# Kernel tuning notes

Hardware: AMD Instinct MI355X
Metric: run time of the kernel (lower is better)

The kernel has to match this reference:

```python
import jax, jax.numpy as jnp
import numpy as np

NB, HD, NL, NF = 5, 64, 4, 10           # num_bins, hidden_dim(d_model), num_layers, num_frames
DI, DS, DC, DTR = 128, 16, 4, 4          # d_inner=2*HD, d_state, d_conv, dt_rank=ceil(HD/16)
B, H, W = 4, 64, 64


def _conv2d(x, w, b):
    y = jax.lax.conv_general_dilated(x, w, (1, 1), 'SAME',
                                     dimension_numbers=('NCHW', 'OIHW', 'NCHW'))
    return y + b[None, :, None, None]


def _bn_relu(x, gamma, beta, eps=1e-5):
    # BatchNorm2d in training mode: biased batch stats over (N,H,W)
    mean = x.mean(axis=(0, 2, 3), keepdims=True)
    var = x.var(axis=(0, 2, 3), keepdims=True)
    y = (x - mean) * jax.lax.rsqrt(var + eps)
    return jax.nn.relu(y * gamma[None, :, None, None] + beta[None, :, None, None])


def _silu(x):
    return x * jax.nn.sigmoid(x)


def _causal_dwconv(x, w, b):
    # x: (B,L,DI), w: (DI,K) depthwise causal conv, b: (DI,)
    K = w.shape[1]
    L = x.shape[1]
    xp = jnp.pad(x, ((0, 0), (K - 1, 0), (0, 0)))
    y = sum(xp[:, k:k + L, :] * w[:, k] for k in range(K))
    return y + b


def _selective_scan(u, delta, A, Bm, Cm, D):
    # u,delta: (B,L,DI); A: (DI,DS); Bm,Cm: (B,L,DS); D: (DI,)
    dT, BT, CT, uT = (t.transpose(1, 0, 2) for t in (delta, Bm, Cm, u))
    h0 = jnp.zeros((u.shape[0], A.shape[0], A.shape[1]), u.dtype)

    def step(h, inp):
        d_t, B_t, C_t, u_t = inp                     # (B,DI),(B,DS),(B,DS),(B,DI)
        dA = jnp.exp(d_t[:, :, None] * A)            # (B,DI,DS)
        h = dA * h + (d_t * u_t)[:, :, None] * B_t[:, None, :]
        y = jnp.einsum('bds,bs->bd', h, C_t)
        return h, y

    _, ys = jax.lax.scan(step, h0, (dT, BT, CT, uT))  # ys: (L,B,DI)
    return ys.transpose(1, 0, 2) + u * D


def _mamba(x, in_proj, conv_w, conv_b, x_proj, dt_w, dt_b, A_log, Dp, out_proj):
    xz = x @ in_proj.T                               # (B,L,2*DI)
    xi, z = jnp.split(xz, 2, axis=-1)
    xi = _silu(_causal_dwconv(xi, conv_w, conv_b))
    xdbc = xi @ x_proj.T                             # (B,L,DTR+2*DS)
    dt, Bm, Cm = jnp.split(xdbc, [DTR, DTR + DS], axis=-1)
    delta = jax.nn.softplus(dt @ dt_w.T + dt_b)
    A = -jnp.exp(A_log)
    y = _selective_scan(xi, delta, A, Bm, Cm, Dp)
    return (y * _silu(z)) @ out_proj.T


def setup_inputs() -> dict:
    key = jax.random.key(0)
    ks = jax.random.split(key, 20)
    s = 0.02
    inp = {
        'x': jax.random.normal(ks[0], (B, NB, H, W), jnp.float32),
        'enc_w': jax.random.normal(ks[1], (HD, NB, 3, 3), jnp.float32) * s,
        'enc_b': jnp.zeros((HD,), jnp.float32),
        'enc_g': jnp.ones((HD,), jnp.float32),
        'enc_be': jnp.zeros((HD,), jnp.float32),
        'in_proj': jax.random.normal(ks[2], (NL, 2 * DI, HD), jnp.float32) * s,
        'conv_w': jax.random.normal(ks[3], (NL, DI, DC), jnp.float32) * s,
        'conv_b': jnp.zeros((NL, DI), jnp.float32),
        'x_proj': jax.random.normal(ks[4], (NL, DTR + 2 * DS, DI), jnp.float32) * s,
        'dt_w': jax.random.normal(ks[5], (NL, DI, DTR), jnp.float32) * s,
        'dt_b': jax.random.normal(ks[6], (NL, DI), jnp.float32) * 0.1 - 4.0,
        'A_log': jnp.broadcast_to(jnp.log(jnp.arange(1, DS + 1, dtype=jnp.float32)),
                                  (NL, DI, DS)).copy(),
        'Dp': jnp.ones((NL, DI), jnp.float32),
        'out_proj': jax.random.normal(ks[7], (NL, HD, DI), jnp.float32) * s,
        'dec1_w': jax.random.normal(ks[8], (HD, HD, 3, 3), jnp.float32) * s,
        'dec1_b': jnp.zeros((HD,), jnp.float32),
        'dec1_g': jnp.ones((HD,), jnp.float32),
        'dec1_be': jnp.zeros((HD,), jnp.float32),
        'dec2_w': jax.random.normal(ks[9], (NF, HD, 3, 3), jnp.float32) * s,
        'dec2_b': jnp.zeros((NF,), jnp.float32),
    }
    return inp


def reference(x, enc_w, enc_b, enc_g, enc_be, in_proj, conv_w, conv_b, x_proj,
              dt_w, dt_b, A_log, Dp, out_proj, dec1_w, dec1_b, dec1_g, dec1_be,
              dec2_w, dec2_b):
    Bb, _, Hh, Ww = x.shape
    h = _bn_relu(_conv2d(x, enc_w, enc_b), enc_g, enc_be)   # (B,HD,H,W)
    t = h.reshape(Bb, HD, Hh * Ww).transpose(0, 2, 1)        # (B,L,HD)
    for i in range(NL):
        t = t + _mamba(t, in_proj[i], conv_w[i], conv_b[i], x_proj[i],
                       dt_w[i], dt_b[i], A_log[i], Dp[i], out_proj[i])
    h = t.transpose(0, 2, 1).reshape(Bb, HD, Hh, Ww)
    h = _bn_relu(_conv2d(h, dec1_w, dec1_b), dec1_g, dec1_be)
    return _conv2d(h, dec2_w, dec2_b)                        # (B,NF,H,W)
```

## Files before the change

kernel.cpp:

```cpp
#include <hip/hip_runtime.h>
#include <hip/hip_bf16.h>

#define BB   4
#define NBC  5
#define HD   64
#define NLAYER 4
#define NFC  10
#define DIM  128
#define DSN  16
#define DCN  4
#define DTRK 4
#define HH   64
#define WWD  64
#define LL   4096
#define MM   (BB*LL)
#define NCHUNK 128
#define CLEN   32
#define TSTEP  16

__global__ void k_prep_all(const float* __restrict__ in_proj, const float* __restrict__ out_proj,
                           const float* __restrict__ dec1_w, const float* __restrict__ dec2_w,
                           float* __restrict__ wTin, float* __restrict__ wTout,
                           float* __restrict__ wT1, float* __restrict__ wT2,
                           float* __restrict__ stats, float* __restrict__ stats2) {
    int idx = blockIdx.x * blockDim.x + threadIdx.x;
    if (idx < 65536) {
        int n = idx & 255, k = (idx >> 8) & 63, l = idx >> 14;
        wTin[idx] = in_proj[(l << 14) + (n << 6) + k];
    } else if (idx < 98304) {
        int j = idx - 65536;
        int n = j & 63, k = (j >> 6) & 127, l = j >> 13;
        wTout[j] = out_proj[(l << 13) + (n << 7) + k];
    } else if (idx < 135168) {
        int j = idx - 98304;
        int co = j & 63, tap = (j >> 6) % 9, ci = j / 576;
        wT1[j] = dec1_w[co * 576 + ci * 9 + tap];
    } else if (idx < 142848) {
        int j = idx - 135168;
        int tap = j % 12, t2 = j / 12, co = t2 % NFC, ci = t2 / NFC;
        wT2[j] = (tap < 9) ? dec2_w[co * 576 + ci * 9 + tap] : 0.f;
    } else if (idx < 143104) {
        int j = idx - 142848;
        if (j < 128) stats[j] = 0.f; else stats2[j - 128] = 0.f;
    }
}

__global__ void k_enc_conv(const float* __restrict__ x, const float* __restrict__ w,
                           const float* __restrict__ bias, float* __restrict__ out,
                           float* __restrict__ stats) {
    __shared__ float r1[256], r2[256];
    int tid = threadIdx.x;
    int idx = blockIdx.x * 256 + tid;
    int wx = idx & 63;
    int hy = (idx >> 6) & 63;
    int co = (idx >> 12) & 63;
    int b  = idx >> 18;
    float acc = bias[co];
    for (int ci = 0; ci < NBC; ++ci) {
        const float* xin = x + (((long)(b * NBC + ci)) << 12);
        const float* wp  = w + (co * NBC + ci) * 9;
        #pragma unroll
        for (int kh = 0; kh < 3; ++kh) {
            int ih = hy + kh - 1;
            if (ih < 0 || ih >= HH) continue;
            #pragma unroll
            for (int kw = 0; kw < 3; ++kw) {
                int iw = wx + kw - 1;
                if (iw < 0 || iw >= WWD) continue;
                acc += xin[(ih << 6) + iw] * wp[kh * 3 + kw];
            }
        }
    }
    out[idx] = acc;
    r1[tid] = acc; r2[tid] = acc * acc;
    __syncthreads();
    for (int off = 128; off > 0; off >>= 1) {
        if (tid < off) { r1[tid] += r1[tid + off]; r2[tid] += r2[tid + off]; }
        __syncthreads();
    }
    if (tid == 0) {
        atomicAdd(&stats[co], r1[0]);
        atomicAdd(&stats[64 + co], r2[0]);
    }
}

__global__ __launch_bounds__(256, 1) void k_gemm_in_bn(const float* __restrict__ src,
                                                       const float* __restrict__ stats,
                                                       const float* __restrict__ g,
                                                       const float* __restrict__ be,
                                                       const float* __restrict__ wT,
                                                       float* __restrict__ tout,
                                                       float* __restrict__ xz) {
    __shared__ __align__(16) float ts[64 * 68];
    __shared__ float sc[64], sh[64];
    long m0 = (long)blockIdx.x << 6;
    int b = (int)(m0 >> 12);
    int hw0 = (int)(m0 & 4095);
    int tid = threadIdx.x;
    if (tid < 64) {
        float m = stats[tid] * (1.f / 16384.f);
        float var = stats[64 + tid] * (1.f / 16384.f) - m * m;
        float ss = g[tid] * rsqrtf(var + 1e-5f);
        sc[tid] = ss; sh[tid] = be[tid] - m * ss;
    }
    __syncthreads();
    for (int i = tid; i < 4096; i += 256) {
        int pix = i & 63, c = i >> 6;
        float v = src[(((long)((b << 6) + c)) << 12) + hw0 + pix];
        ts[pix * 68 + c] = fmaxf(v * sc[c] + sh[c], 0.f);
    }
    __syncthreads();
    for (int i = tid; i < 4096; i += 256) {
        int r = i >> 6, c = i & 63;
        tout[(m0 + r) * 64 + c] = ts[r * 68 + c];
    }
    int rg = tid >> 5;
    int cg = tid & 31;
    float acc[8][8] = {};
    int n0 = cg << 3;
    for (int k4 = 0; k4 < 16; ++k4) {
        float4 a[8];
        #pragma unroll
        for (int r2 = 0; r2 < 8; ++r2)
            a[r2] = *(const float4*)&ts[((rg << 3) + r2) * 68 + (k4 << 2)];
        #pragma unroll
        for (int kk = 0; kk < 4; ++kk) {
            const float* wr = wT + (((k4 << 2) + kk) << 8) + n0;
            float4 w0 = *(const float4*)&wr[0];
            float4 w1 = *(const float4*)&wr[4];
            #pragma unroll
            for (int r2 = 0; r2 < 8; ++r2) {
                float av = (kk == 0) ? a[r2].x : (kk == 1) ? a[r2].y
                         : (kk == 2) ? a[r2].z : a[r2].w;
                acc[r2][0] += av * w0.x; acc[r2][1] += av * w0.y;
                acc[r2][2] += av * w0.z; acc[r2][3] += av * w0.w;
                acc[r2][4] += av * w1.x; acc[r2][5] += av * w1.y;
                acc[r2][6] += av * w1.z; acc[r2][7] += av * w1.w;
            }
        }
    }
    #pragma unroll
    for (int r2 = 0; r2 < 8; ++r2) {
        long m = m0 + (rg << 3) + r2;
        *(float4*)&xz[(m << 8) + n0]     = make_float4(acc[r2][0], acc[r2][1], acc[r2][2], acc[r2][3]);
        *(float4*)&xz[(m << 8) + n0 + 4] = make_float4(acc[r2][4], acc[r2][5], acc[r2][6], acc[r2][7]);
    }
}

__global__ __launch_bounds__(256, 2) void k_xproj_fused(
        const float* __restrict__ xz, const float* __restrict__ cw,
        const float* __restrict__ cb, const float* __restrict__ Wx,
        const float* __restrict__ dw, const float* __restrict__ dbias,
        const float* __restrict__ A_log,
        float* __restrict__ xi, float* __restrict__ xdbc,
        float* __restrict__ delta, float* __restrict__ Pb, float* __restrict__ Sb) {
    __shared__ float xz_s[35 * 132];
    __shared__ float xi_s[32 * 132];
    __shared__ float w_s[36 * 132];
    __shared__ float xs[32 * 40];
    __shared__ float cwT[4 * 128];
    __shared__ float cb_s[128];
    long m0 = (long)blockIdx.x << 5;
    int l0 = (int)(m0 & 4095);
    int b = (int)(m0 >> 12);
    int chunk = l0 >> 5;
    int tid = threadIdx.x;

    for (int i = tid; i < 35 * 128; i += 256) {
        int j = i >> 7, k = i & 127;
        int l = l0 - 3 + j;
        float v = 0.f;
        if (l >= 0) v = xz[(m0 - 3 + j) * 256 + k];
        xz_s[j * 132 + k] = v;
    }
    if (tid < 128) cb_s[tid] = cb[tid];
    for (int i = tid; i < 512; i += 256) {
        int kk = i >> 7, di = i & 127;
        cwT[(kk << 7) + di] = cw[(di << 2) + kk];
    }
    for (int i = tid; i < 4608; i += 256) {
        int n = i >> 7, k = i & 127;
        w_s[n * 132 + k] = Wx[i];
    }
    __syncthreads();

    for (int ii = 0; ii < 4; ++ii) {
        int i = tid + (ii << 8);
        int r = i >> 5;
        int d4 = (i & 31) << 2;
        float4 a = *(const float4*)&cb_s[d4];
        #pragma unroll
        for (int kk = 0; kk < 4; ++kk) {
            float4 xv = *(const float4*)&xz_s[(r + kk) * 132 + d4];
            float4 wv = *(const float4*)&cwT[(kk << 7) + d4];
            a.x += xv.x * wv.x; a.y += xv.y * wv.y;
            a.z += xv.z * wv.z; a.w += xv.w * wv.w;
        }
        a.x = a.x / (1.f + __expf(-a.x));
        a.y = a.y / (1.f + __expf(-a.y));
        a.z = a.z / (1.f + __expf(-a.z));
        a.w = a.w / (1.f + __expf(-a.w));
        *(float4*)&xi_s[r * 132 + d4] = a;
        *(float4*)&xi[(m0 + r) * 128 + d4] = a;
    }
    __syncthreads();

    int n = tid & 63;
    int rg = tid >> 6;
    if (n < 36) {
        float acc[8] = {0,0,0,0,0,0,0,0};
        for (int k4 = 0; k4 < 32; ++k4) {
            float4 w4 = *(const float4*)&w_s[n * 132 + (k4 << 2)];
            #pragma unroll
            for (int r = 0; r < 8; ++r) {
                float4 a4 = *(const float4*)&xi_s[((rg << 3) + r) * 132 + (k4 << 2)];
                acc[r] += a4.x * w4.x + a4.y * w4.y + a4.z * w4.z + a4.w * w4.w;
            }
        }
        #pragma unroll
        for (int r = 0; r < 8; ++r) {
            int rr = (rg << 3) + r;
            xdbc[(m0 + rr) * 36 + n] = acc[r];
            xs[rr * 40 + n] = acc[r];
        }
    }
    __syncthreads();

    float* delta_s = xz_s;
    for (int i = tid; i < 4096; i += 256) {
        int r = i >> 7, di = i & 127;
        float v = dbias[di];
        float4 d4 = *(const float4*)&dw[di << 2];
        v += xs[r * 40 + 0] * d4.x + xs[r * 40 + 1] * d4.y
           + xs[r * 40 + 2] * d4.z + xs[r * 40 + 3] * d4.w;
        float sp = (v > 20.f) ? v : log1pf(expf(v));
        delta[(m0 + r) * 128 + di] = sp;
        delta_s[r * 132 + di] = sp;
    }
    __syncthreads();

    {
        int di = tid >> 1;
        int dso = (tid & 1) << 3;
        float4 al0 = *(const float4*)&A_log[(di << 4) + dso];
        float4 al1 = *(const float4*)&A_log[(di << 4) + dso + 4];
        float Av[8] = { -expf(al0.x), -expf(al0.y), -expf(al0.z), -expf(al0.w),
                        -expf(al1.x), -expf(al1.y), -expf(al1.z), -expf(al1.w) };
        float h[8] = {0,0,0,0,0,0,0,0};
        float P[8] = {1,1,1,1,1,1,1,1};
        #pragma unroll 4
        for (int i = 0; i < CLEN; ++i) {
            float d = delta_s[i * 132 + di];
            float u = xi_s[i * 132 + di];
            float du = d * u;
            float4 B0 = *(float4*)&xs[i * 40 + DTRK + dso];
            float4 B1 = *(float4*)&xs[i * 40 + DTRK + dso + 4];
            float a0 = __expf(d * Av[0]); h[0] = a0 * h[0] + du * B0.x; P[0] *= a0;
            float a1 = __expf(d * Av[1]); h[1] = a1 * h[1] + du * B0.y; P[1] *= a1;
            float a2 = __expf(d * Av[2]); h[2] = a2 * h[2] + du * B0.z; P[2] *= a2;
            float a3 = __expf(d * Av[3]); h[3] = a3 * h[3] + du * B0.w; P[3] *= a3;
            float a4 = __expf(d * Av[4]); h[4] = a4 * h[4] + du * B1.x; P[4] *= a4;
            float a5 = __expf(d * Av[5]); h[5] = a5 * h[5] + du * B1.y; P[5] *= a5;
            float a6 = __expf(d * Av[6]); h[6] = a6 * h[6] + du * B1.z; P[6] *= a6;
            float a7 = __expf(d * Av[7]); h[7] = a7 * h[7] + du * B1.w; P[7] *= a7;
        }
        long o = (((long)chunk * BB + b) << 11) + (di << 4) + dso;
        *(float4*)&Pb[o]     = make_float4(P[0], P[1], P[2], P[3]);
        *(float4*)&Pb[o + 4] = make_float4(P[4], P[5], P[6], P[7]);
        *(float4*)&Sb[o]     = make_float4(h[0], h[1], h[2], h[3]);
        *(float4*)&Sb[o + 4] = make_float4(h[4], h[5], h[6], h[7]);
    }
}

__global__ void k_scan_p2(float* Pb, const float* __restrict__ Sb) {
    int t = blockIdx.x * blockDim.x + threadIdx.x;
    int b = t >> 11;
    int s = t & 2047;
    float h = 0.f;
    for (int c = 0; c < NCHUNK; ++c) {
        long idx = (((long)c * BB + b) << 11) + s;
        float p = Pb[idx];
        float sv = Sb[idx];
        Pb[idx] = h;
        h = p * h + sv;
    }
}

__global__ __launch_bounds__(256, 1) void k_scan_p3_oi(
        const float* __restrict__ delta, const float* __restrict__ xi,
        const float* __restrict__ xdbc, const float* __restrict__ A_log,
        const float* __restrict__ Dp, const float* __restrict__ xz,
        const float* __restrict__ hin, const float* __restrict__ wTo,
        const float* __restrict__ wTi, float* __restrict__ tio,
        float* __restrict__ xz_out, int doB) {
    __shared__ __align__(16) float d_s[32 * 132];
    __shared__ __align__(16) float u_s[32 * 132];
    __shared__ __align__(16) float bc_s[32 * 36];
    __shared__ __align__(16) float t_s[32 * 68];
    int chunk = blockIdx.x, b = blockIdx.y;
    int tid = threadIdx.x;
    long t0 = ((long)b << 12) + (long)chunk * CLEN;

    for (int i = tid; i < 1024; i += 256) {
        int r = i >> 5, c4 = (i & 31) << 2;
        *(float4*)&d_s[r * 132 + c4] = *(const float4*)&delta[(t0 + r) * 128 + c4];
        *(float4*)&u_s[r * 132 + c4] = *(const float4*)&xi[(t0 + r) * 128 + c4];
    }
    {
        int r = tid >> 3, c4 = (tid & 7) << 2;
        *(float4*)&bc_s[r * 36 + c4] = *(const float4*)&xdbc[(t0 + r) * 36 + DTRK + c4];
    }

    int di = tid >> 1;
    int dso = (tid & 1) << 3;
    float4 al0 = *(const float4*)&A_log[(di << 4) + dso];
    float4 al1 = *(const float4*)&A_log[(di << 4) + dso + 4];
    float Av[8] = { -expf(al0.x), -expf(al0.y), -expf(al0.z), -expf(al0.w),
                    -expf(al1.x), -expf(al1.y), -expf(al1.z), -expf(al1.w) };
    float Dv = Dp[di];
    long o = (((long)chunk * BB + b) << 11) + (di << 4) + dso;
    float4 h0 = *(const float4*)&hin[o];
    float4 h1 = *(const float4*)&hin[o + 4];
    float h[8] = { h0.x, h0.y, h0.z, h0.w, h1.x, h1.y, h1.z, h1.w };
    __syncthreads();

    #pragma unroll 4
    for (int i = 0; i < CLEN; ++i) {
        float d = d_s[i * 132 + di];
        float u = u_s[i * 132 + di];
        float du = d * u;
        const float* bc = &bc_s[i * 36];
        float4 B0 = *(const float4*)&bc[dso];
        float4 B1 = *(const float4*)&bc[dso + 4];
        float4 C0 = *(const float4*)&bc[16 + dso];
        float4 C1 = *(const float4*)&bc[16 + dso + 4];
        float a0 = __expf(d * Av[0]); h[0] = a0 * h[0] + du * B0.x;
        float a1 = __expf(d * Av[1]); h[1] = a1 * h[1] + du * B0.y;
        float a2 = __expf(d * Av[2]); h[2] = a2 * h[2] + du * B0.z;
        float a3 = __expf(d * Av[3]); h[3] = a3 * h[3] + du * B0.w;
        float a4 = __expf(d * Av[4]); h[4] = a4 * h[4] + du * B1.x;
        float a5 = __expf(d * Av[5]); h[5] = a5 * h[5] + du * B1.y;
        float a6 = __expf(d * Av[6]); h[6] = a6 * h[6] + du * B1.z;
        float a7 = __expf(d * Av[7]); h[7] = a7 * h[7] + du * B1.w;
        float yp = h[0] * C0.x + h[1] * C0.y + h[2] * C0.z + h[3] * C0.w
                 + h[4] * C1.x + h[5] * C1.y + h[6] * C1.z + h[7] * C1.w;
        yp += __shfl_xor(yp, 1);
        if (dso == 0)
            u_s[i * 132 + di] = yp + u * Dv;
    }
    __syncthreads();

    for (int i = tid; i < 1024; i += 256) {
        int r = i >> 5, c4 = (i & 31) << 2;
        float4 y4 = *(float4*)&u_s[r * 132 + c4];
        float4 z4 = *(const float4*)&xz[((t0 + r) << 8) + DIM + c4];
        y4.x *= z4.x / (1.f + __expf(-z4.x));
        y4.y *= z4.y / (1.f + __expf(-z4.y));
        y4.z *= z4.z / (1.f + __expf(-z4.z));
        y4.w *= z4.w / (1.f + __expf(-z4.w));
        *(float4*)&u_s[r * 132 + c4] = y4;
    }
    __syncthreads();

    {
        int rg = tid >> 4, cg = tid & 15;
        int n0 = cg << 2;
        float acc[2][4] = {};
        for (int k4 = 0; k4 < 32; ++k4) {
            float4 a0 = *(const float4*)&u_s[(rg << 1) * 132 + (k4 << 2)];
            float4 a1 = *(const float4*)&u_s[((rg << 1) + 1) * 132 + (k4 << 2)];
            #pragma unroll
            for (int kk = 0; kk < 4; ++kk) {
                const float* wr = wTo + (((k4 << 2) + kk) << 6) + n0;
                float4 w0 = *(const float4*)&wr[0];
                float av0 = (kk == 0) ? a0.x : (kk == 1) ? a0.y : (kk == 2) ? a0.z : a0.w;
                float av1 = (kk == 0) ? a1.x : (kk == 1) ? a1.y : (kk == 2) ? a1.z : a1.w;
                acc[0][0] += av0 * w0.x; acc[0][1] += av0 * w0.y;
                acc[0][2] += av0 * w0.z; acc[0][3] += av0 * w0.w;
                acc[1][0] += av1 * w0.x; acc[1][1] += av1 * w0.y;
                acc[1][2] += av1 * w0.z; acc[1][3] += av1 * w0.w;
            }
        }
        #pragma unroll
        for (int r2 = 0; r2 < 2; ++r2) {
            long m = t0 + (rg << 1) + r2;
            float4 tv = *(const float4*)&tio[(m << 6) + n0];
            tv.x += acc[r2][0]; tv.y += acc[r2][1];
            tv.z += acc[r2][2]; tv.w += acc[r2][3];
            *(float4*)&tio[(m << 6) + n0] = tv;
            *(float4*)&t_s[((rg << 1) + r2) * 68 + n0] = tv;
        }
    }
    if (!doB) return;
    __syncthreads();

    {
        int rg = tid >> 5, cgn = tid & 31;
        int n0 = cgn << 3;
        float acc[4][8] = {};
        for (int k4 = 0; k4 < 16; ++k4) {
            float4 a[4];
            #pragma unroll
            for (int r2 = 0; r2 < 4; ++r2)
                a[r2] = *(const float4*)&t_s[((rg << 2) + r2) * 68 + (k4 << 2)];
            #pragma unroll
            for (int kk = 0; kk < 4; ++kk) {
                const float* wr = wTi + (((k4 << 2) + kk) << 8) + n0;
                float4 w0 = *(const float4*)&wr[0];
                float4 w1 = *(const float4*)&wr[4];
                #pragma unroll
                for (int r2 = 0; r2 < 4; ++r2) {
                    float av = (kk == 0) ? a[r2].x : (kk == 1) ? a[r2].y
                             : (kk == 2) ? a[r2].z : a[r2].w;
                    acc[r2][0] += av * w0.x; acc[r2][1] += av * w0.y;
                    acc[r2][2] += av * w0.z; acc[r2][3] += av * w0.w;
                    acc[r2][4] += av * w1.x; acc[r2][5] += av * w1.y;
                    acc[r2][6] += av * w1.z; acc[r2][7] += av * w1.w;
                }
            }
        }
        #pragma unroll
        for (int r2 = 0; r2 < 4; ++r2) {
            long m = t0 + (rg << 2) + r2;
            *(float4*)&xz_out[(m << 8) + n0]     = make_float4(acc[r2][0], acc[r2][1], acc[r2][2], acc[r2][3]);
            *(float4*)&xz_out[(m << 8) + n0 + 4] = make_float4(acc[r2][4], acc[r2][5], acc[r2][6], acc[r2][7]);
        }
    }
}

__global__ __launch_bounds__(256, 1) void k_dec1_new(const float* __restrict__ tin,
                                                     const float* __restrict__ wT,
                                                     const float* __restrict__ bias,
                                                     float* __restrict__ out,
                                                     float* __restrict__ stats2) {
    __shared__ __align__(16) float x_s[64 * 132];
    __shared__ __align__(16) float w_s[4 * 4608];
    int tile = blockIdx.x;
    int b = blockIdx.y;
    int ty0 = (tile >> 3) << 3;
    int tx0 = (tile & 7) << 3;
    int tid = threadIdx.x;
    int wv = tid >> 6;
    int lane = tid & 63;
    int r = lane >> 3;
    int cg = lane & 7;

    for (int i = tid; i < 6400; i += 256) {
        int pl = i >> 6;
        int c = i & 63;
        int py = pl / 10, px = pl - py * 10;
        int ih = ty0 + py - 1, iw = tx0 + px - 1;
        float v = 0.f;
        if (ih >= 0 && ih < HH && iw >= 0 && iw < WWD)
            v = tin[(((long)((b << 12) + (ih << 6) + iw)) << 6) + c];
        x_s[c * 132 + py * 12 + px] = v;
    }
    float* myw = &w_s[wv * 4608];
    const float* gw = wT + (wv * 16) * 576;
    float4 pref[18];
    #pragma unroll
    for (int i = 0; i < 18; ++i)
        pref[i] = *(const float4*)&gw[(i * 64 + lane) * 4];
    #pragma unroll
    for (int i = 0; i < 18; ++i)
        *(float4*)&myw[(i * 64 + lane) * 4] = pref[i];
    __syncthreads();

    float acc[8][8] = {};
    #pragma unroll
    for (int ch = 0; ch < 2; ++ch) {
        if (ch == 0) {
            const float* gw1 = wT + (wv * 16 + 8) * 576;
            #pragma unroll
            for (int i = 0; i < 18; ++i)
                pref[i] = *(const float4*)&gw1[(i * 64 + lane) * 4];
        }
        for (int cl = 0; cl < 8; ++cl) {
            int cib = wv * 16 + ch * 8 + cl;
            float xrow[3][10];
            #pragma unroll
            for (int kh = 0; kh < 3; ++kh) {
                const float* xr = &x_s[cib * 132 + (r + kh) * 12];
                float4 a0 = *(const float4*)&xr[0];
                float4 a1 = *(const float4*)&xr[4];
                float2 a2 = *(const float2*)&xr[8];
                xrow[kh][0] = a0.x; xrow[kh][1] = a0.y; xrow[kh][2] = a0.z; xrow[kh][3] = a0.w;
                xrow[kh][4] = a1.x; xrow[kh][5] = a1.y; xrow[kh][6] = a1.z; xrow[kh][7] = a1.w;
                xrow[kh][8] = a2.x; xrow[kh][9] = a2.y;
            }
            const float* wp = &myw[cl * 576];
            #pragma unroll
            for (int kh = 0; kh < 3; ++kh) {
                #pragma unroll
                for (int kw = 0; kw < 3; ++kw) {
                    const float* wp2 = wp + (kh * 3 + kw) * 64 + (cg << 3);
                    float4 wa = *(const float4*)&wp2[0];
                    float4 wb = *(const float4*)&wp2[4];
                    #pragma unroll
                    for (int j = 0; j < 8; ++j) {
                        float xv = xrow[kh][kw + j];
                        acc[j][0] += xv * wa.x; acc[j][1] += xv * wa.y;
                        acc[j][2] += xv * wa.z; acc[j][3] += xv * wa.w;
                        acc[j][4] += xv * wb.x; acc[j][5] += xv * wb.y;
                        acc[j][6] += xv * wb.z; acc[j][7] += xv * wb.w;
                    }
                }
            }
        }
        if (ch == 0) {
            #pragma unroll
            for (int i = 0; i < 18; ++i)
                *(float4*)&myw[(i * 64 + lane) * 4] = pref[i];
        }
    }

    #pragma unroll
    for (int j = 0; j < 8; ++j) {
        *(float4*)&myw[lane * 68 + (j << 3)]     = make_float4(acc[j][0], acc[j][1], acc[j][2], acc[j][3]);
        *(float4*)&myw[lane * 68 + (j << 3) + 4] = make_float4(acc[j][4], acc[j][5], acc[j][6], acc[j][7]);
    }
    __syncthreads();

    float bv = bias[lane];
    float ssum = 0.f, ssq = 0.f;
    #pragma unroll
    for (int pp = 0; pp < 16; ++pp) {
        int pr = (wv << 1) + (pp >> 3);
        int pc = pp & 7;
        int ol = (pr << 3) + (lane >> 3);
        int ix = (pc << 3) + (lane & 7);
        float s = w_s[ol * 68 + ix] + w_s[4608 + ol * 68 + ix]
                + w_s[9216 + ol * 68 + ix] + w_s[13824 + ol * 68 + ix] + bv;
        out[(((long)((b << 12) + ((ty0 + pr) << 6) + tx0 + pc)) << 6) + lane] = s;
        ssum += s; ssq += s * s;
    }
    float* red = x_s;
    red[(wv << 6) + lane] = ssum;
    red[256 + (wv << 6) + lane] = ssq;
    __syncthreads();
    if (tid < 64) {
        float a = red[tid] + red[64 + tid] + red[128 + tid] + red[192 + tid];
        float q = red[256 + tid] + red[320 + tid] + red[384 + tid] + red[448 + tid];
        atomicAdd(&stats2[tid], a);
        atomicAdd(&stats2[64 + tid], q);
    }
}

__global__ void k_dec2_fused(const float* __restrict__ src, const float* __restrict__ stats2,
                             const float* __restrict__ g, const float* __restrict__ be,
                             const float* __restrict__ wT, const float* __restrict__ bias,
                             float* __restrict__ out) {
    __shared__ float x_s[64 * 101];
    __shared__ float w_s[64 * NFC * 12];
    __shared__ float sc_s[64];
    __shared__ float sh_s[64];
    int tile = blockIdx.x;
    int b = blockIdx.y;
    int ty0 = (tile >> 3) << 3;
    int tx0 = (tile & 7) << 3;
    int tid = threadIdx.x;

    if (tid < 64) {
        float m = stats2[tid] * (1.f / 16384.f);
        float var = stats2[64 + tid] * (1.f / 16384.f) - m * m;
        float s = g[tid] * rsqrtf(var + 1e-5f);
        sc_s[tid] = s;
        sh_s[tid] = be[tid] - m * s;
    }
    for (int i = tid; i < 64 * NFC * 12; i += 256)
        w_s[i] = wT[i];
    __syncthreads();

    for (int i = tid; i < 6400; i += 256) {
        int pl = i >> 6;
        int c = i & 63;
        int py = pl / 10, px = pl - py * 10;
        int ih = ty0 + py - 1, iw = tx0 + px - 1;
        float v = 0.f;
        if (ih >= 0 && ih < HH && iw >= 0 && iw < WWD) {
            v = src[((long)((b << 12) + (ih << 6) + iw)) * 64 + c];
            v = fmaxf(v * sc_s[c] + sh_s[c], 0.f);
        }
        x_s[c * 101 + pl] = v;
    }
    __syncthreads();

    int px = tid & 63;
    int py = px >> 3, pxx = px & 7;
    int cog = tid >> 6;
    float acc[3] = {0.f, 0.f, 0.f};
    int nco = (cog < 2) ? 3 : 2;

    for (int ci = 0; ci < 64; ++ci) {
        const float* xr = &x_s[ci * 101 + py * 10 + pxx];
        float xv[9];
        #pragma unroll
        for (int kh = 0; kh < 3; ++kh)
            #pragma unroll
            for (int kw = 0; kw < 3; ++kw)
                xv[kh * 3 + kw] = xr[kh * 10 + kw];
        #pragma unroll
        for (int j = 0; j < 3; ++j) {
            if (j >= nco) break;
            int co = cog + (j << 2);
            const float* wp = &w_s[(ci * NFC + co) * 12];
            float4 w0 = *(const float4*)&wp[0];
            float4 w1 = *(const float4*)&wp[4];
            float  w8 = wp[8];
            acc[j] += xv[0] * w0.x + xv[1] * w0.y + xv[2] * w0.z + xv[3] * w0.w
                    + xv[4] * w1.x + xv[5] * w1.y + xv[6] * w1.z + xv[7] * w1.w
                    + xv[8] * w8;
        }
    }
    int hw = ((ty0 + py) << 6) + tx0 + pxx;
    #pragma unroll
    for (int j = 0; j < 3; ++j) {
        if (j >= nco) break;
        int co = cog + (j << 2);
        out[((long)(b * NFC + co) << 12) + hw] = acc[j] + bias[co];
    }
}

extern "C" void kernel_launch(void* const* d_in, const int* in_sizes, int n_in,
                              void* d_out, int out_size, void* d_ws, size_t ws_size,
                              hipStream_t stream) {
    const float* x       = (const float*)d_in[0];
    const float* enc_w   = (const float*)d_in[1];
    const float* enc_b   = (const float*)d_in[2];
    const float* enc_g   = (const float*)d_in[3];
    const float* enc_be  = (const float*)d_in[4];
    const float* in_proj = (const float*)d_in[5];
    const float* conv_w  = (const float*)d_in[6];
    const float* conv_b  = (const float*)d_in[7];
    const float* x_proj  = (const float*)d_in[8];
    const float* dt_w    = (const float*)d_in[9];
    const float* dt_b    = (const float*)d_in[10];
    const float* A_log   = (const float*)d_in[11];
    const float* Dp      = (const float*)d_in[12];
    const float* out_prj = (const float*)d_in[13];
    const float* dec1_w  = (const float*)d_in[14];
    const float* dec1_b  = (const float*)d_in[15];
    const float* dec1_g  = (const float*)d_in[16];
    const float* dec1_be = (const float*)d_in[17];
    const float* dec2_w  = (const float*)d_in[18];
    const float* dec2_b  = (const float*)d_in[19];
    float* out = (float*)d_out;

    float* ws = (float*)d_ws;
    size_t off = 0;
    float* conv_buf  = ws + off; off += 1048576;
    float* stats     = ws + off; off += 128;
    float* stats2    = ws + off; off += 128;
    float* wT1       = ws + off; off += 36864;
    float* wT2       = ws + off; off += 7680;
    float* wTin      = ws + off; off += 65536;
    float* wTout     = ws + off; off += 32768;
    float* t_buf     = ws + off; off += 1048576;
    float* xz_buf    = ws + off; off += 4194304;
    float* xi_buf    = ws + off; off += 2097152;
    float* xdbc_buf  = ws + off; off += 589824;
    float* delta_buf = ws + off; off += 2097152;
    float* Sb_buf    = ws + off; off += 1048576;
    (void)ws_size; (void)in_sizes; (void)n_in; (void)out_size;

    float* Pb = conv_buf;
    float* Sb = Sb_buf;

    k_prep_all<<<560, 256, 0, stream>>>(in_proj, out_prj, dec1_w, dec2_w,
                                        wTin, wTout, wT1, wT2, stats, stats2);

    k_enc_conv<<<4096, 256, 0, stream>>>(x, enc_w, enc_b, conv_buf, stats);

    k_gemm_in_bn<<<256, 256, 0, stream>>>(conv_buf, stats, enc_g, enc_be, wTin, t_buf, xz_buf);
    dim3 pg(NCHUNK, BB);
    for (int i = 0; i < NLAYER; ++i) {
        k_xproj_fused<<<512, 256, 0, stream>>>(xz_buf, conv_w + i * DIM * DCN,
                                               conv_b + i * DIM, x_proj + i * 36 * DIM,
                                               dt_w + i * DIM * DTRK, dt_b + i * DIM,
                                               A_log + i * DIM * DSN,
                                               xi_buf, xdbc_buf, delta_buf, Pb, Sb);
        k_scan_p2<<<32, 256, 0, stream>>>(Pb, Sb);
        int doB = (i < NLAYER - 1) ? 1 : 0;
        k_scan_p3_oi<<<pg, 256, 0, stream>>>(delta_buf, xi_buf, xdbc_buf,
                                             A_log + i * DIM * DSN, Dp + i * DIM,
                                             xz_buf, Pb, wTout + i * 8192,
                                             wTin + ((i + 1) & 3) * 16384,
                                             t_buf, xz_buf, doB);
    }

    dim3 dg1(64, BB);
    k_dec1_new<<<dg1, 256, 0, stream>>>(t_buf, wT1, dec1_b, conv_buf, stats2);
    k_dec2_fused<<<dg1, 256, 0, stream>>>(conv_buf, stats2, dec1_g, dec1_be, wT2, dec2_b, out);
}
```

Before: 490.9 us.

## Double threads per block in xproj and scan-p3 kernels, halving per-thread work

```diff
diff --git a/kernel.cpp b/kernel.cpp
--- a/kernel.cpp
+++ b/kernel.cpp
@@ -147,7 +147,7 @@
     }
 }
 
-__global__ __launch_bounds__(256, 2) void k_xproj_fused(
+__global__ __launch_bounds__(512, 4) void k_xproj_fused(
         const float* __restrict__ xz, const float* __restrict__ cw,
         const float* __restrict__ cb, const float* __restrict__ Wx,
         const float* __restrict__ dw, const float* __restrict__ dbias,
@@ -166,7 +166,7 @@
     int chunk = l0 >> 5;
     int tid = threadIdx.x;
 
-    for (int i = tid; i < 35 * 128; i += 256) {
+    for (int i = tid; i < 35 * 128; i += 512) {
         int j = i >> 7, k = i & 127;
         int l = l0 - 3 + j;
         float v = 0.f;
@@ -174,18 +174,19 @@
         xz_s[j * 132 + k] = v;
     }
     if (tid < 128) cb_s[tid] = cb[tid];
-    for (int i = tid; i < 512; i += 256) {
-        int kk = i >> 7, di = i & 127;
-        cwT[(kk << 7) + di] = cw[(di << 2) + kk];
-    }
-    for (int i = tid; i < 4608; i += 256) {
+    {
+        int kk = tid >> 7, di = tid & 127;
+        if (tid < 512) cwT[(kk << 7) + di] = cw[(di << 2) + kk];
+    }
+    for (int i = tid; i < 4608; i += 512) {
         int n = i >> 7, k = i & 127;
         w_s[n * 132 + k] = Wx[i];
     }
     __syncthreads();
 
-    for (int ii = 0; ii < 4; ++ii) {
-        int i = tid + (ii << 8);
+    #pragma unroll
+    for (int ii = 0; ii < 2; ++ii) {
+        int i = tid + (ii << 9);
         int r = i >> 5;
         int d4 = (i & 31) << 2;
         float4 a = *(const float4*)&cb_s[d4];
@@ -208,18 +209,18 @@
     int n = tid & 63;
     int rg = tid >> 6;
     if (n < 36) {
-        float acc[8] = {0,0,0,0,0,0,0,0};
+        float acc[4] = {0, 0, 0, 0};
         for (int k4 = 0; k4 < 32; ++k4) {
             float4 w4 = *(const float4*)&w_s[n * 132 + (k4 << 2)];
             #pragma unroll
-            for (int r = 0; r < 8; ++r) {
-                float4 a4 = *(const float4*)&xi_s[((rg << 3) + r) * 132 + (k4 << 2)];
+            for (int r = 0; r < 4; ++r) {
+                float4 a4 = *(const float4*)&xi_s[((rg << 2) + r) * 132 + (k4 << 2)];
                 acc[r] += a4.x * w4.x + a4.y * w4.y + a4.z * w4.z + a4.w * w4.w;
             }
         }
         #pragma unroll
-        for (int r = 0; r < 8; ++r) {
-            int rr = (rg << 3) + r;
+        for (int r = 0; r < 4; ++r) {
+            int rr = (rg << 2) + r;
             xdbc[(m0 + rr) * 36 + n] = acc[r];
             xs[rr * 40 + n] = acc[r];
         }
@@ -227,7 +228,7 @@
     __syncthreads();
 
     float* delta_s = xz_s;
-    for (int i = tid; i < 4096; i += 256) {
+    for (int i = tid; i < 4096; i += 512) {
         int r = i >> 7, di = i & 127;
         float v = dbias[di];
         float4 d4 = *(const float4*)&dw[di << 2];
@@ -240,35 +241,26 @@
     __syncthreads();
 
     {
-        int di = tid >> 1;
-        int dso = (tid & 1) << 3;
-        float4 al0 = *(const float4*)&A_log[(di << 4) + dso];
-        float4 al1 = *(const float4*)&A_log[(di << 4) + dso + 4];
-        float Av[8] = { -expf(al0.x), -expf(al0.y), -expf(al0.z), -expf(al0.w),
-                        -expf(al1.x), -expf(al1.y), -expf(al1.z), -expf(al1.w) };
-        float h[8] = {0,0,0,0,0,0,0,0};
-        float P[8] = {1,1,1,1,1,1,1,1};
+        int di = tid >> 2;
+        int dso = (tid & 3) << 2;
+        float4 al = *(const float4*)&A_log[(di << 4) + dso];
+        float Av[4] = { -expf(al.x), -expf(al.y), -expf(al.z), -expf(al.w) };
+        float h[4] = {0, 0, 0, 0};
+        float P[4] = {1, 1, 1, 1};
         #pragma unroll 4
         for (int i = 0; i < CLEN; ++i) {
             float d = delta_s[i * 132 + di];
             float u = xi_s[i * 132 + di];
             float du = d * u;
             float4 B0 = *(float4*)&xs[i * 40 + DTRK + dso];
-            float4 B1 = *(float4*)&xs[i * 40 + DTRK + dso + 4];
             float a0 = __expf(d * Av[0]); h[0] = a0 * h[0] + du * B0.x; P[0] *= a0;
             float a1 = __expf(d * Av[1]); h[1] = a1 * h[1] + du * B0.y; P[1] *= a1;
             float a2 = __expf(d * Av[2]); h[2] = a2 * h[2] + du * B0.z; P[2] *= a2;
             float a3 = __expf(d * Av[3]); h[3] = a3 * h[3] + du * B0.w; P[3] *= a3;
-            float a4 = __expf(d * Av[4]); h[4] = a4 * h[4] + du * B1.x; P[4] *= a4;
-            float a5 = __expf(d * Av[5]); h[5] = a5 * h[5] + du * B1.y; P[5] *= a5;
-            float a6 = __expf(d * Av[6]); h[6] = a6 * h[6] + du * B1.z; P[6] *= a6;
-            float a7 = __expf(d * Av[7]); h[7] = a7 * h[7] + du * B1.w; P[7] *= a7;
         }
         long o = (((long)chunk * BB + b) << 11) + (di << 4) + dso;
-        *(float4*)&Pb[o]     = make_float4(P[0], P[1], P[2], P[3]);
-        *(float4*)&Pb[o + 4] = make_float4(P[4], P[5], P[6], P[7]);
-        *(float4*)&Sb[o]     = make_float4(h[0], h[1], h[2], h[3]);
-        *(float4*)&Sb[o + 4] = make_float4(h[4], h[5], h[6], h[7]);
+        *(float4*)&Pb[o] = make_float4(P[0], P[1], P[2], P[3]);
+        *(float4*)&Sb[o] = make_float4(h[0], h[1], h[2], h[3]);
     }
 }
 
@@ -286,7 +278,7 @@
     }
 }
 
-__global__ __launch_bounds__(256, 1) void k_scan_p3_oi(
+__global__ __launch_bounds__(512, 4) void k_scan_p3_oi(
         const float* __restrict__ delta, const float* __restrict__ xi,
         const float* __restrict__ xdbc, const float* __restrict__ A_log,
         const float* __restrict__ Dp, const float* __restrict__ xz,
@@ -301,27 +293,24 @@
     int tid = threadIdx.x;
     long t0 = ((long)b << 12) + (long)chunk * CLEN;
 
-    for (int i = tid; i < 1024; i += 256) {
+    for (int i = tid; i < 1024; i += 512) {
         int r = i >> 5, c4 = (i & 31) << 2;
         *(float4*)&d_s[r * 132 + c4] = *(const float4*)&delta[(t0 + r) * 128 + c4];
         *(float4*)&u_s[r * 132 + c4] = *(const float4*)&xi[(t0 + r) * 128 + c4];
     }
-    {
+    if (tid < 256) {
         int r = tid >> 3, c4 = (tid & 7) << 2;
         *(float4*)&bc_s[r * 36 + c4] = *(const float4*)&xdbc[(t0 + r) * 36 + DTRK + c4];
     }
 
-    int di = tid >> 1;
-    int dso = (tid & 1) << 3;
-    float4 al0 = *(const float4*)&A_log[(di << 4) + dso];
-    float4 al1 = *(const float4*)&A_log[(di << 4) + dso + 4];
-    float Av[8] = { -expf(al0.x), -expf(al0.y), -expf(al0.z), -expf(al0.w),
-                    -expf(al1.x), -expf(al1.y), -expf(al1.z), -expf(al1.w) };
+    int di = tid >> 2;
+    int dso = (tid & 3) << 2;
+    float4 al = *(const float4*)&A_log[(di << 4) + dso];
+    float Av[4] = { -expf(al.x), -expf(al.y), -expf(al.z), -expf(al.w) };
     float Dv = Dp[di];
     long o = (((long)chunk * BB + b) << 11) + (di << 4) + dso;
     float4 h0 = *(const float4*)&hin[o];
-    float4 h1 = *(const float4*)&hin[o + 4];
-    float h[8] = { h0.x, h0.y, h0.z, h0.w, h1.x, h1.y, h1.z, h1.w };
+    float h[4] = { h0.x, h0.y, h0.z, h0.w };
     __syncthreads();
 
     #pragma unroll 4
@@ -331,26 +320,20 @@
         float du = d * u;
         const float* bc = &bc_s[i * 36];
         float4 B0 = *(const float4*)&bc[dso];
-        float4 B1 = *(const float4*)&bc[dso + 4];
         float4 C0 = *(const float4*)&bc[16 + dso];
-        float4 C1 = *(const float4*)&bc[16 + dso + 4];
         float a0 = __expf(d * Av[0]); h[0] = a0 * h[0] + du * B0.x;
         float a1 = __expf(d * Av[1]); h[1] = a1 * h[1] + du * B0.y;
         float a2 = __expf(d * Av[2]); h[2] = a2 * h[2] + du * B0.z;
         float a3 = __expf(d * Av[3]); h[3] = a3 * h[3] + du * B0.w;
-        float a4 = __expf(d * Av[4]); h[4] = a4 * h[4] + du * B1.x;
-        float a5 = __expf(d * Av[5]); h[5] = a5 * h[5] + du * B1.y;
-        float a6 = __expf(d * Av[6]); h[6] = a6 * h[6] + du * B1.z;
-        float a7 = __expf(d * Av[7]); h[7] = a7 * h[7] + du * B1.w;
-        float yp = h[0] * C0.x + h[1] * C0.y + h[2] * C0.z + h[3] * C0.w
-                 + h[4] * C1.x + h[5] * C1.y + h[6] * C1.z + h[7] * C1.w;
+        float yp = h[0] * C0.x + h[1] * C0.y + h[2] * C0.z + h[3] * C0.w;
         yp += __shfl_xor(yp, 1);
+        yp += __shfl_xor(yp, 2);
         if (dso == 0)
             u_s[i * 132 + di] = yp + u * Dv;
     }
     __syncthreads();
 
-    for (int i = tid; i < 1024; i += 256) {
+    for (int i = tid; i < 1024; i += 512) {
         int r = i >> 5, c4 = (i & 31) << 2;
         float4 y4 = *(float4*)&u_s[r * 132 + c4];
         float4 z4 = *(const float4*)&xz[((t0 + r) << 8) + DIM + c4];
@@ -365,31 +348,24 @@
     {
         int rg = tid >> 4, cg = tid & 15;
         int n0 = cg << 2;
-        float acc[2][4] = {};
+        float acc4[4] = {};
         for (int k4 = 0; k4 < 32; ++k4) {
-            float4 a0 = *(const float4*)&u_s[(rg << 1) * 132 + (k4 << 2)];
-            float4 a1 = *(const float4*)&u_s[((rg << 1) + 1) * 132 + (k4 << 2)];
+            float4 a0 = *(const float4*)&u_s[rg * 132 + (k4 << 2)];
             #pragma unroll
             for (int kk = 0; kk < 4; ++kk) {
                 const float* wr = wTo + (((k4 << 2) + kk) << 6) + n0;
                 float4 w0 = *(const float4*)&wr[0];
-                float av0 = (kk == 0) ? a0.x : (kk == 1) ? a0.y : (kk == 2) ? a0.z : a0.w;
-                float av1 = (kk == 0) ? a1.x : (kk == 1) ? a1.y : (kk == 2) ? a1.z : a1.w;
-                acc[0][0] += av0 * w0.x; acc[0][1] += av0 * w0.y;
-                acc[0][2] += av0 * w0.z; acc[0][3] += av0 * w0.w;
-                acc[1][0] += av1 * w0.x; acc[1][1] += av1 * w0.y;
-                acc[1][2] += av1 * w0.z; acc[1][3] += av1 * w0.w;
+                float av = (kk == 0) ? a0.x : (kk == 1) ? a0.y : (kk == 2) ? a0.z : a0.w;
+                acc4[0] += av * w0.x; acc4[1] += av * w0.y;
+                acc4[2] += av * w0.z; acc4[3] += av * w0.w;
             }
         }
-        #pragma unroll
-        for (int r2 = 0; r2 < 2; ++r2) {
-            long m = t0 + (rg << 1) + r2;
-            float4 tv = *(const float4*)&tio[(m << 6) + n0];
-            tv.x += acc[r2][0]; tv.y += acc[r2][1];
-            tv.z += acc[r2][2]; tv.w += acc[r2][3];
-            *(float4*)&tio[(m << 6) + n0] = tv;
-            *(float4*)&t_s[((rg << 1) + r2) * 68 + n0] = tv;
-        }
+        long m = t0 + rg;
+        float4 tv = *(const float4*)&tio[(m << 6) + n0];
+        tv.x += acc4[0]; tv.y += acc4[1];
+        tv.z += acc4[2]; tv.w += acc4[3];
+        *(float4*)&tio[(m << 6) + n0] = tv;
+        *(float4*)&t_s[rg * 68 + n0] = tv;
     }
     if (!doB) return;
     __syncthreads();
@@ -397,19 +373,18 @@
     {
         int rg = tid >> 5, cgn = tid & 31;
         int n0 = cgn << 3;
-        float acc[4][8] = {};
+        float acc[2][8] = {};
         for (int k4 = 0; k4 < 16; ++k4) {
-            float4 a[4];
-            #pragma unroll
-            for (int r2 = 0; r2 < 4; ++r2)
-                a[r2] = *(const float4*)&t_s[((rg << 2) + r2) * 68 + (k4 << 2)];
+            float4 a[2];
+            a[0] = *(const float4*)&t_s[(rg << 1) * 68 + (k4 << 2)];
+            a[1] = *(const float4*)&t_s[((rg << 1) + 1) * 68 + (k4 << 2)];
             #pragma unroll
             for (int kk = 0; kk < 4; ++kk) {
                 const float* wr = wTi + (((k4 << 2) + kk) << 8) + n0;
                 float4 w0 = *(const float4*)&wr[0];
                 float4 w1 = *(const float4*)&wr[4];
                 #pragma unroll
-                for (int r2 = 0; r2 < 4; ++r2) {
+                for (int r2 = 0; r2 < 2; ++r2) {
                     float av = (kk == 0) ? a[r2].x : (kk == 1) ? a[r2].y
                              : (kk == 2) ? a[r2].z : a[r2].w;
                     acc[r2][0] += av * w0.x; acc[r2][1] += av * w0.y;
@@ -420,8 +395,8 @@
             }
         }
         #pragma unroll
-        for (int r2 = 0; r2 < 4; ++r2) {
-            long m = t0 + (rg << 2) + r2;
+        for (int r2 = 0; r2 < 2; ++r2) {
+            long m = t0 + (rg << 1) + r2;
             *(float4*)&xz_out[(m << 8) + n0]     = make_float4(acc[r2][0], acc[r2][1], acc[r2][2], acc[r2][3]);
             *(float4*)&xz_out[(m << 8) + n0 + 4] = make_float4(acc[r2][4], acc[r2][5], acc[r2][6], acc[r2][7]);
         }
@@ -674,14 +649,14 @@
     k_gemm_in_bn<<<256, 256, 0, stream>>>(conv_buf, stats, enc_g, enc_be, wTin, t_buf, xz_buf);
     dim3 pg(NCHUNK, BB);
     for (int i = 0; i < NLAYER; ++i) {
-        k_xproj_fused<<<512, 256, 0, stream>>>(xz_buf, conv_w + i * DIM * DCN,
+        k_xproj_fused<<<512, 512, 0, stream>>>(xz_buf, conv_w + i * DIM * DCN,
                                                conv_b + i * DIM, x_proj + i * 36 * DIM,
                                                dt_w + i * DIM * DTRK, dt_b + i * DIM,
                                                A_log + i * DIM * DSN,
                                                xi_buf, xdbc_buf, delta_buf, Pb, Sb);
         k_scan_p2<<<32, 256, 0, stream>>>(Pb, Sb);
         int doB = (i < NLAYER - 1) ? 1 : 0;
-        k_scan_p3_oi<<<pg, 256, 0, stream>>>(delta_buf, xi_buf, xdbc_buf,
+        k_scan_p3_oi<<<pg, 512, 0, stream>>>(delta_buf, xi_buf, xdbc_buf,
                                              A_log + i * DIM * DSN, Dp + i * DIM,
                                              xz_buf, Pb, wTout + i * 8192,
                                              wTin + ((i + 1) & 3) * 16384,
```

New measurement: 520.8 us. 1.06x slower.
